# Optimization experiments

Hardware: AMD Instinct MI355X
Metric: run time of the kernel (lower is better)

## Reference

```python
import jax, jax.numpy as jnp
import numpy as np

B, S, E, H = 4, 2048, 1024, 16
D = E // H
SCALE = np.sqrt(D).astype(np.float32)


def setup_inputs() -> dict:
    key = jax.random.key(0)
    ks = jax.random.split(key, 9)
    s = 1.0 / np.sqrt(E)
    return {
        "x": jax.random.normal(ks[0], (B, S, E), dtype=jnp.float32),
        "Wq": jax.random.uniform(ks[1], (E, E), jnp.float32, -s, s),
        "bq": jax.random.uniform(ks[2], (E,), jnp.float32, -s, s),
        "Wk": jax.random.uniform(ks[3], (E, E), jnp.float32, -s, s),
        "bk": jax.random.uniform(ks[4], (E,), jnp.float32, -s, s),
        "Wv": jax.random.uniform(ks[5], (E, E), jnp.float32, -s, s),
        "bv": jax.random.uniform(ks[6], (E,), jnp.float32, -s, s),
        "Wo": jax.random.uniform(ks[7], (E, E), jnp.float32, -s, s),
        "bo": jax.random.uniform(ks[8], (E,), jnp.float32, -s, s),
    }


def reference(x, Wq, bq, Wk, bk, Wv, bv, Wo, bo):
    # Linear projections (torch Linear: y = x @ W.T + b)
    q = x @ Wq.T + bq  # [B,S,E]
    k = x @ Wk.T + bk
    v = x @ Wv.T + bv
    # split heads -> [B,H,S,D]
    q = q.reshape(B, S, H, D).transpose(0, 2, 1, 3)
    k = k.reshape(B, S, H, D).transpose(0, 2, 1, 3)
    v = v.reshape(B, S, H, D).transpose(0, 2, 1, 3)
    scores = jnp.einsum("bhqd,bhkd->bhqk", q, k) / SCALE  # [B,H,S,S]
    attn = jax.nn.softmax(scores, axis=-1)  # dropout is identity at inference
    out = jnp.einsum("bhqk,bhkd->bhqd", attn, v)  # [B,H,S,D]
    out = out.transpose(0, 2, 1, 3).reshape(B, S, E)
    return out @ Wo.T + bo
```

## Files before the change

kernel.cpp:

```cpp
#include <hip/hip_runtime.h>
#include <math.h>

#define Bb 4
#define Ss 2048
#define Ee 1024
#define Hh 16
#define Dd 64

static constexpr int Mtot = Bb * Ss;
static constexpr size_t NK = (size_t)Ee * Ee;

typedef __bf16 bf16x8 __attribute__((ext_vector_type(8)));
typedef float  f32x16 __attribute__((ext_vector_type(16)));
typedef unsigned int uint32x2 __attribute__((ext_vector_type(2)));

extern "C" __device__ float __ocml_native_exp2_f32(float);

#define AS1(p) ((const __attribute__((address_space(1))) void*)(p))
#define AS3(p) ((__attribute__((address_space(3))) void*)(p))

__device__ __forceinline__ unsigned short rne1(float x) {
  unsigned u = __float_as_uint(x);
  return (unsigned short)((u + 0x7FFFu + ((u >> 16) & 1u)) >> 16);
}
__device__ __forceinline__ short4 rne4(const float4 v) {
  short4 r;
  r.x = (short)rne1(v.x); r.y = (short)rne1(v.y);
  r.z = (short)rne1(v.z); r.w = (short)rne1(v.w);
  return r;
}

__global__ __launch_bounds__(256) void prep(const float* __restrict__ x,
                                            const float* __restrict__ wq,
                                            const float* __restrict__ wk,
                                            const float* __restrict__ wv,
                                            const float* __restrict__ wo,
                                            unsigned short* __restrict__ xb,
                                            unsigned short* __restrict__ wqkv,
                                            unsigned short* __restrict__ wob) {
  const int X4 = (int)((size_t)Mtot * Ee / 4);
  const int W4 = (int)(NK / 4);
  const int i = blockIdx.x * 256 + threadIdx.x;
  const float* src;
  unsigned short* dst;
  int off;
  if (i < X4) {
    src = x; dst = xb; off = i;
  } else {
    const int j = i - X4;
    const int seg = j >> 18;
    off = j & (W4 - 1);
    if (seg == 0)      { src = wq; dst = wqkv; }
    else if (seg == 1) { src = wk; dst = wqkv + NK; }
    else if (seg == 2) { src = wv; dst = wqkv + 2 * NK; }
    else               { src = wo; dst = wob; }
  }
  float4 v = ((const float4*)src)[off];
  ((short4*)dst)[off] = rne4(v);
}

__device__ __forceinline__ void gemm_core(const unsigned short* __restrict__ A,
                                          const unsigned short* __restrict__ W,
                                          unsigned short* sm, int bm, int bn,
                                          int tid, f32x16 acc[2][2]) {
  unsigned short* sA = sm;
  unsigned short* sW = sm + 8192;
  const int lane = tid & 63, w = tid >> 6;
  const int wm = (w & 1) << 6, wn = (w >> 1) << 6;
  const int m32 = lane & 31, g = lane >> 5;
  const int sw = m32 & 7;

  const int srow = (w << 5) + (lane >> 3);
  const int scol = ((lane & 7) ^ (lane >> 3)) << 3;
  const unsigned short* Ag = A + (size_t)(bm + srow) * Ee + scol;
  const unsigned short* Wg = W + (size_t)(bn + srow) * Ee + scol;
  unsigned short* sAw = sA + (w << 11);
  unsigned short* sWw = sW + (w << 11);

  for (int k0 = 0; k0 < Ee; k0 += 64) {
    __syncthreads();
#pragma unroll
    for (int i = 0; i < 4; ++i) {
      __builtin_amdgcn_global_load_lds(AS1(Ag + (size_t)(i << 3) * Ee + k0),
                                       AS3(sAw + (i << 9)), 16, 0, 0);
      __builtin_amdgcn_global_load_lds(AS1(Wg + (size_t)(i << 3) * Ee + k0),
                                       AS3(sWw + (i << 9)), 16, 0, 0);
    }
    __syncthreads();
#pragma unroll
    for (int kk = 0; kk < 64; kk += 16) {
      const int ch = (((kk >> 3) | g) ^ sw) << 3;
      bf16x8 af[2], wf[2];
#pragma unroll
      for (int s = 0; s < 2; ++s) {
        af[s] = *(const bf16x8*)(sA + ((wm + (s << 5) + m32) << 6) + ch);
        wf[s] = *(const bf16x8*)(sW + ((wn + (s << 5) + m32) << 6) + ch);
      }
#pragma unroll
      for (int si = 0; si < 2; ++si)
#pragma unroll
        for (int sj = 0; sj < 2; ++sj)
          acc[si][sj] = __builtin_amdgcn_mfma_f32_32x32x16_bf16(af[si], wf[sj], acc[si][sj], 0, 0, 0);
    }
  }
}


__global__ __launch_bounds__(256) void gemm_qkv(const unsigned short* __restrict__ xb,
                                                const unsigned short* __restrict__ wqkv,
                                                const float* __restrict__ bq,
                                                const float* __restrict__ bk,
                                                const float* __restrict__ bv,
                                                unsigned short* __restrict__ Qb,
                                                unsigned short* __restrict__ Kb,
                                                unsigned short* __restrict__ Vt) {
  __shared__ unsigned short sm[16384];
  f32x16 acc[2][2] = {};
  const int tid = threadIdx.x;
  const int bm = blockIdx.x << 7, bn = blockIdx.y << 7;
  gemm_core(xb, wqkv, sm, bm, bn, tid, acc);

  const int lane = tid & 63, w = tid >> 6;
  const int wm = (w & 1) << 6, wn = (w >> 1) << 6;
  const int m32 = lane & 31, g = lane >> 5;
  const int proj = blockIdx.y >> 3;
  const int cb   = (blockIdx.y & 7) << 7;
  const float* bp = proj == 0 ? bq : (proj == 1 ? bk : bv);
  const float SC = 0.18033688011112042f;

  if (proj == 2) {
    const int bmS = bm & (Ss - 1);
    const int b = bm >> 11;
#pragma unroll
    for (int si = 0; si < 2; ++si)
#pragma unroll
      for (int sj = 0; sj < 2; ++sj) {
        const int col = cb + wn + (sj << 5) + m32;
        const int hh = col >> 6, dd = col & 63;
        const float bvv = bp[col];
        unsigned short* vrow = Vt + ((size_t)((b * Hh + hh) * Dd + dd)) * Ss;
#pragma unroll
        for (int rq = 0; rq < 4; ++rq) {
          const int s0 = bmS + wm + (si << 5) + (g << 2) + (rq << 3);
          float4 v;
          v.x = acc[si][sj][rq * 4 + 0] + bvv;
          v.y = acc[si][sj][rq * 4 + 1] + bvv;
          v.z = acc[si][sj][rq * 4 + 2] + bvv;
          v.w = acc[si][sj][rq * 4 + 3] + bvv;
          *(short4*)(vrow + s0) = rne4(v);
        }
      }
  } else {
    unsigned short* dst = proj == 0 ? Qb : Kb;
    const float sc = proj == 0 ? SC : 1.0f;
#pragma unroll
    for (int si = 0; si < 2; ++si)
#pragma unroll
      for (int sj = 0; sj < 2; ++sj) {
        const int col = cb + wn + (sj << 5) + m32;
        const int hh = col >> 6, dd = col & 63;
        const float bvv = bp[col];
#pragma unroll
        for (int reg = 0; reg < 16; ++reg) {
          const int row = bm + wm + (si << 5) + (g << 2) + (reg & 3) + ((reg >> 2) << 3);
          const int b = row >> 11, s = row & (Ss - 1);
          dst[((size_t)((b * Hh + hh) * Ss + s)) * Dd + dd] =
              rne1((acc[si][sj][reg] + bvv) * sc);
        }
      }
  }
}

__global__ __launch_bounds__(256) void gemm_out(const unsigned short* __restrict__ Ab,
                                                const unsigned short* __restrict__ Wb,
                                                const float* __restrict__ bias,
                                                float* __restrict__ C) {
  __shared__ unsigned short sm[16384];
  f32x16 acc[2][2] = {};
  const int tid = threadIdx.x;
  const int bm = blockIdx.x << 7, bn = blockIdx.y << 7;
  gemm_core(Ab, Wb, sm, bm, bn, tid, acc);
  const int lane = tid & 63, w = tid >> 6;
  const int wm = (w & 1) << 6, wn = (w >> 1) << 6;
  const int m32 = lane & 31, g = lane >> 5;
#pragma unroll
  for (int si = 0; si < 2; ++si)
#pragma unroll
    for (int sj = 0; sj < 2; ++sj) {
      const int col = bn + wn + (sj << 5) + m32;
      const float bv = bias[col];
#pragma unroll
      for (int reg = 0; reg < 16; ++reg) {
        const int row = bm + wm + (si << 5) + (g << 2) + (reg & 3) + ((reg >> 2) << 3);
        C[(size_t)row * Ee + col] = acc[si][sj][reg] + bv;
      }
    }
}

__global__ __launch_bounds__(256) void flash_mfma(const unsigned short* __restrict__ Qb,
                                                  const unsigned short* __restrict__ Kb,
                                                  const unsigned short* __restrict__ Vt,
                                                  unsigned short* __restrict__ Ob) {
  __shared__ unsigned short smem[9216];
  unsigned short* Kh = smem;
  unsigned short* Vh = smem + 4608;
  const int tid = threadIdx.x;
  const int lane = tid & 63, w = tid >> 6;
  const int m32 = lane & 31, g = lane >> 5;
  const int qt = blockIdx.x << 7;
  const int bh = blockIdx.y;

  const size_t ph = (size_t)bh * Ss * Dd;
  const unsigned short* qp = Qb + ph + (size_t)(qt + (w << 5) + m32) * Dd + (g << 3);
  bf16x8 qf[4];
#pragma unroll
  for (int c = 0; c < 4; ++c) qf[c] = *(const bf16x8*)(qp + (c << 4));

  const int sr = tid >> 2;
  const int sc = (tid & 3) << 4;
  const unsigned short* kg = Kb + ph + (size_t)sr * Dd + sc;
  const unsigned short* vg = Vt + (size_t)bh * Dd * Ss + (size_t)sr * Ss + sc;
  const int so = sr * 72 + sc;

  uint4 k0 = *(const uint4*)(kg);
  uint4 k1 = *(const uint4*)(kg + 8);
  uint4 v0 = *(const uint4*)(vg);
  uint4 v1 = *(const uint4*)(vg + 8);

  f32x16 acc_o[2] = {};
  float l_ = 0.f;

  for (int kt = 0; kt < Ss; kt += 64) {
    __syncthreads();
    *(uint4*)(&Kh[so]) = k0; *(uint4*)(&Kh[so + 8]) = k1;
    *(uint4*)(&Vh[so]) = v0; *(uint4*)(&Vh[so + 8]) = v1;
    __syncthreads();
    if (kt + 64 < Ss) {
      const unsigned short* kg2 = kg + (size_t)(kt + 64) * Dd;
      const unsigned short* vg2 = vg + (kt + 64);
      k0 = *(const uint4*)(kg2);
      k1 = *(const uint4*)(kg2 + 8);
      v0 = *(const uint4*)(vg2);
      v1 = *(const uint4*)(vg2 + 8);
    }

    float p[2][16];
#pragma unroll
    for (int mt = 0; mt < 2; ++mt) {
      f32x16 a = {};
#pragma unroll
      for (int c = 0; c < 4; ++c) {
        bf16x8 kf = *(const bf16x8*)(&Kh[((mt << 5) + m32) * 72 + (c << 4) + (g << 3)]);
        a = __builtin_amdgcn_mfma_f32_32x32x16_bf16(kf, qf[c], a, 0, 0, 0);
      }
#pragma unroll
      for (int r = 0; r < 16; ++r) p[mt][r] = a[r];
    }
    float rs = 0.f;
#pragma unroll
    for (int mt = 0; mt < 2; ++mt)
#pragma unroll
      for (int r = 0; r < 16; ++r) {
        float e = __ocml_native_exp2_f32(p[mt][r]);
        e = __uint_as_float(__float_as_uint(e) & 0xFFFF0000u);
        p[mt][r] = e;
        rs += e;
      }
    rs += __shfl_xor(rs, 32);
    l_ += rs;

#pragma unroll
    for (int c = 0; c < 4; ++c) {
      const int mt = c >> 1, b8 = (c & 1) << 3;
      unsigned dw0 = __builtin_amdgcn_perm(__float_as_uint(p[mt][b8 + 1]), __float_as_uint(p[mt][b8 + 0]), 0x07060302u);
      unsigned dw1 = __builtin_amdgcn_perm(__float_as_uint(p[mt][b8 + 3]), __float_as_uint(p[mt][b8 + 2]), 0x07060302u);
      unsigned dw2 = __builtin_amdgcn_perm(__float_as_uint(p[mt][b8 + 5]), __float_as_uint(p[mt][b8 + 4]), 0x07060302u);
      unsigned dw3 = __builtin_amdgcn_perm(__float_as_uint(p[mt][b8 + 7]), __float_as_uint(p[mt][b8 + 6]), 0x07060302u);
      const uint32x2 s02 = __builtin_amdgcn_permlane32_swap(dw0, dw2, false, false);
      const uint32x2 s13 = __builtin_amdgcn_permlane32_swap(dw1, dw3, false, false);
      union { unsigned u[4]; bf16x8 v; } pf;
      pf.u[0] = s02[0];
      pf.u[1] = s13[0];
      pf.u[2] = s02[1];
      pf.u[3] = s13[1];
#pragma unroll
      for (int dt = 0; dt < 2; ++dt) {
        bf16x8 vf = *(const bf16x8*)(&Vh[((dt << 5) + m32) * 72 + (c << 4) + (g << 3)]);
        acc_o[dt] = __builtin_amdgcn_mfma_f32_32x32x16_bf16(vf, pf.v, acc_o[dt], 0, 0, 0);
      }
    }
  }

  const float inv = 1.0f / l_;
  const int q = (w << 5) + m32;
  unsigned short* Of = smem;
  __syncthreads();
#pragma unroll
  for (int dt = 0; dt < 2; ++dt)
#pragma unroll
    for (int r = 0; r < 16; ++r) {
      const int d = (dt << 5) + (g << 2) + (r & 3) + ((r >> 2) << 3);
      Of[q * 72 + d] = rne1(acc_o[dt][r] * inv);
    }
  __syncthreads();
  const int orow = tid >> 1, oc = (tid & 1) << 5;
  const int bq = bh >> 4, hh = bh & 15;
  const size_t obase = ((size_t)(bq * Ss + qt + orow)) * Ee + hh * Dd + oc;
#pragma unroll
  for (int i = 0; i < 2; ++i)
    *(uint4*)(Ob + obase + (i << 3)) = *(const uint4*)(&Of[orow * 72 + oc + (i << 3)]);
#pragma unroll
  for (int i = 2; i < 4; ++i)
    *(uint4*)(Ob + obase + (i << 3)) = *(const uint4*)(&Of[orow * 72 + oc + (i << 3)]);
}

extern "C" void kernel_launch(void* const* d_in, const int* in_sizes, int n_in,
                              void* d_out, int out_size, void* d_ws, size_t ws_size,
                              hipStream_t stream) {
  const float* x  = (const float*)d_in[0];
  const float* Wq = (const float*)d_in[1];
  const float* bq = (const float*)d_in[2];
  const float* Wk = (const float*)d_in[3];
  const float* bk = (const float*)d_in[4];
  const float* Wv = (const float*)d_in[5];
  const float* bv = (const float*)d_in[6];
  const float* Wo = (const float*)d_in[7];
  const float* bo = (const float*)d_in[8];
  float* out = (float*)d_out;

  const size_t nX = (size_t)Mtot * Ee;
  unsigned short* xb   = (unsigned short*)d_ws;
  unsigned short* qb   = xb + nX;
  unsigned short* kb   = qb + nX;
  unsigned short* vt   = kb + nX;
  unsigned short* ob   = vt + nX;
  unsigned short* wqkv = ob + nX;
  unsigned short* wob  = wqkv + 3 * NK;

  const int total4 = (int)(nX / 4 + NK);
  prep<<<total4 / 256, 256, 0, stream>>>(x, Wq, Wk, Wv, Wo, xb, wqkv, wob);

  gemm_qkv<<<dim3(Mtot / 128, 3 * Ee / 128), 256, 0, stream>>>(xb, wqkv, bq, bk, bv, qb, kb, vt);

  flash_mfma<<<dim3(Ss / 128, Bb * Hh), 256, 0, stream>>>(qb, kb, vt, ob);

  gemm_out<<<dim3(Mtot / 128, Ee / 128), 256, 0, stream>>>(ob, wob, bo, out);
}
```

Before: 292.9 us.

## Double-buffer GEMM LDS tiles and compute softmax row sums with MFMA

The shared GEMM core now uses two LDS buffers, so global-to-LDS loads for the next K tile are issued before the MFMAs on the current tile. This is meant to overlap load latency with compute, at the cost of doubling LDS per block (64 KB), which can lower occupancy. In the attention kernel the per-element bf16 truncation, the scalar row-sum adds and the cross-lane shuffle are replaced by an extra MFMA that multiplies the packed probabilities by a ones vector. That moves the denominator work onto the matrix unit and keeps it consistent with the truncated bf16 values fed to the PV MFMA.

```diff
diff --git a/kernel.cpp b/kernel.cpp
--- a/kernel.cpp
+++ b/kernel.cpp
@@ -63,8 +63,6 @@
                                           const unsigned short* __restrict__ W,
                                           unsigned short* sm, int bm, int bn,
                                           int tid, f32x16 acc[2][2]) {
-  unsigned short* sA = sm;
-  unsigned short* sW = sm + 8192;
   const int lane = tid & 63, w = tid >> 6;
   const int wm = (w & 1) << 6, wn = (w >> 1) << 6;
   const int m32 = lane & 31, g = lane >> 5;
@@ -74,19 +72,35 @@
   const int scol = ((lane & 7) ^ (lane >> 3)) << 3;
   const unsigned short* Ag = A + (size_t)(bm + srow) * Ee + scol;
   const unsigned short* Wg = W + (size_t)(bn + srow) * Ee + scol;
-  unsigned short* sAw = sA + (w << 11);
-  unsigned short* sWw = sW + (w << 11);
-
+
+  {
+    unsigned short* sAw = sm + (w << 11);
+    unsigned short* sWw = sm + 8192 + (w << 11);
+#pragma unroll
+    for (int i = 0; i < 4; ++i) {
+      __builtin_amdgcn_global_load_lds(AS1(Ag + (size_t)(i << 3) * Ee),
+                                       AS3(sAw + (i << 9)), 16, 0, 0);
+      __builtin_amdgcn_global_load_lds(AS1(Wg + (size_t)(i << 3) * Ee),
+                                       AS3(sWw + (i << 9)), 16, 0, 0);
+    }
+  }
+  __syncthreads();
+
+  int cur = 0;
   for (int k0 = 0; k0 < Ee; k0 += 64) {
-    __syncthreads();
-#pragma unroll
-    for (int i = 0; i < 4; ++i) {
-      __builtin_amdgcn_global_load_lds(AS1(Ag + (size_t)(i << 3) * Ee + k0),
-                                       AS3(sAw + (i << 9)), 16, 0, 0);
-      __builtin_amdgcn_global_load_lds(AS1(Wg + (size_t)(i << 3) * Ee + k0),
-                                       AS3(sWw + (i << 9)), 16, 0, 0);
-    }
-    __syncthreads();
+    if (k0 + 64 < Ee) {
+      unsigned short* sAw = sm + ((cur ^ 1) << 14) + (w << 11);
+      unsigned short* sWw = sm + ((cur ^ 1) << 14) + 8192 + (w << 11);
+#pragma unroll
+      for (int i = 0; i < 4; ++i) {
+        __builtin_amdgcn_global_load_lds(AS1(Ag + (size_t)(i << 3) * Ee + k0 + 64),
+                                         AS3(sAw + (i << 9)), 16, 0, 0);
+        __builtin_amdgcn_global_load_lds(AS1(Wg + (size_t)(i << 3) * Ee + k0 + 64),
+                                         AS3(sWw + (i << 9)), 16, 0, 0);
+      }
+    }
+    const unsigned short* sA = sm + (cur << 14);
+    const unsigned short* sW = sA + 8192;
 #pragma unroll
     for (int kk = 0; kk < 64; kk += 16) {
       const int ch = (((kk >> 3) | g) ^ sw) << 3;
@@ -102,6 +116,8 @@
         for (int sj = 0; sj < 2; ++sj)
           acc[si][sj] = __builtin_amdgcn_mfma_f32_32x32x16_bf16(af[si], wf[sj], acc[si][sj], 0, 0, 0);
     }
+    __syncthreads();
+    cur ^= 1;
   }
 }
 
@@ -114,7 +130,7 @@
                                                 unsigned short* __restrict__ Qb,
                                                 unsigned short* __restrict__ Kb,
                                                 unsigned short* __restrict__ Vt) {
-  __shared__ unsigned short sm[16384];
+  __shared__ unsigned short sm[32768];
   f32x16 acc[2][2] = {};
   const int tid = threadIdx.x;
   const int bm = blockIdx.x << 7, bn = blockIdx.y << 7;
@@ -175,7 +191,7 @@
                                                 const unsigned short* __restrict__ Wb,
                                                 const float* __restrict__ bias,
                                                 float* __restrict__ C) {
-  __shared__ unsigned short sm[16384];
+  __shared__ unsigned short sm[32768];
   f32x16 acc[2][2] = {};
   const int tid = threadIdx.x;
   const int bm = blockIdx.x << 7, bn = blockIdx.y << 7;
@@ -216,6 +232,11 @@
 #pragma unroll
   for (int c = 0; c < 4; ++c) qf[c] = *(const bf16x8*)(qp + (c << 4));
 
+  union { unsigned short us[8]; bf16x8 v; } onesu;
+#pragma unroll
+  for (int i = 0; i < 8; ++i) onesu.us[i] = 0x3F80;
+  const bf16x8 ones = onesu.v;
+
   const int sr = tid >> 2;
   const int sc = (tid & 3) << 4;
   const unsigned short* kg = Kb + ph + (size_t)sr * Dd + sc;
@@ -228,7 +249,7 @@
   uint4 v1 = *(const uint4*)(vg + 8);
 
   f32x16 acc_o[2] = {};
-  float l_ = 0.f;
+  f32x16 acc_l = {};
 
   for (int kt = 0; kt < Ss; kt += 64) {
     __syncthreads();
@@ -256,18 +277,11 @@
 #pragma unroll
       for (int r = 0; r < 16; ++r) p[mt][r] = a[r];
     }
-    float rs = 0.f;
 #pragma unroll
     for (int mt = 0; mt < 2; ++mt)
 #pragma unroll
-      for (int r = 0; r < 16; ++r) {
-        float e = __ocml_native_exp2_f32(p[mt][r]);
-        e = __uint_as_float(__float_as_uint(e) & 0xFFFF0000u);
-        p[mt][r] = e;
-        rs += e;
-      }
-    rs += __shfl_xor(rs, 32);
-    l_ += rs;
+      for (int r = 0; r < 16; ++r)
+        p[mt][r] = __ocml_native_exp2_f32(p[mt][r]);
 
 #pragma unroll
     for (int c = 0; c < 4; ++c) {
@@ -288,10 +302,11 @@
         bf16x8 vf = *(const bf16x8*)(&Vh[((dt << 5) + m32) * 72 + (c << 4) + (g << 3)]);
         acc_o[dt] = __builtin_amdgcn_mfma_f32_32x32x16_bf16(vf, pf.v, acc_o[dt], 0, 0, 0);
       }
-    }
-  }
-
-  const float inv = 1.0f / l_;
+      acc_l = __builtin_amdgcn_mfma_f32_32x32x16_bf16(ones, pf.v, acc_l, 0, 0, 0);
+    }
+  }
+
+  const float inv = 1.0f / acc_l[0];
   const int q = (w << 5) + m32;
   unsigned short* Of = smem;
   __syncthreads();
```

Result: no change. 288.1 us (-1.6%).
